# Kernel tuning notes

Hardware: AMD Instinct MI355X
Metric: run time of the kernel (lower is better)

Reference implementation:

```python
import jax, jax.numpy as jnp
import numpy as np

N = 200_000      # nodes
E = 6_400_000    # edges (avg degree 32)
ATT = 16         # scorer hidden dim
MAXD = 512       # mixer max_depth
C = 1.0          # curvature
EPS = 1e-15


def _mobius_add(a, b, c):
    # Mobius addition on the Poincare ball: a (+)_c b
    ab = jnp.sum(a * b, axis=-1, keepdims=True)
    aa = jnp.sum(a * a, axis=-1, keepdims=True)
    bb = jnp.sum(b * b, axis=-1, keepdims=True)
    num = (1.0 + 2.0 * c * ab + c * bb) * a + (1.0 - c * aa) * b
    den = 1.0 + 2.0 * c * ab + (c * c) * aa * bb
    return num / jnp.maximum(den, EPS)


def setup_inputs() -> dict:
    key = jax.random.key(0)
    ks = jax.random.split(key, 8)
    x = jax.random.normal(ks[0], (N, 2), dtype=jnp.float32)
    # keep nodes strictly inside the unit Poincare disk (|x| < 0.5)
    x = 0.5 * x / (1.0 + jnp.linalg.norm(x, axis=-1, keepdims=True))
    edge_index = jax.random.randint(ks[1], (2, E), 0, N, dtype=jnp.int32)
    depth = jax.random.randint(ks[2], (N,), 0, MAXD, dtype=jnp.int32)
    W1 = jax.random.normal(ks[3], (2, ATT), dtype=jnp.float32) * (1.0 / np.sqrt(2.0))
    b1 = jnp.zeros((ATT,), dtype=jnp.float32)
    W2 = jax.random.normal(ks[4], (ATT, 1), dtype=jnp.float32) * (1.0 / np.sqrt(ATT))
    eta = jnp.array(1.0, dtype=jnp.float32)
    depth_scale = 1.0 + 0.1 * jax.random.normal(ks[5], (MAXD, 1), dtype=jnp.float32)
    depth_theta = 0.1 * jax.random.normal(ks[6], (MAXD, 1), dtype=jnp.float32)
    return dict(x=x, edge_index=edge_index, depth=depth, W1=W1, b1=b1, W2=W2,
                eta=eta, depth_scale=depth_scale, depth_theta=depth_theta)


def reference(x, edge_index, depth, W1, b1, W2, eta, depth_scale, depth_theta):
    c = C
    sc = jnp.sqrt(jnp.asarray(c, dtype=x.dtype))
    row, col = edge_index[0], edge_index[1]
    xi = x[row]   # [E,2] target node of each edge
    xj = x[col]   # [E,2] source node of each edge

    # log_{xi}(xj): tangent vector at xi
    u = _mobius_add(-xi, xj, c)                                        # [E,2]
    un = jnp.maximum(jnp.linalg.norm(u, axis=-1, keepdims=True), EPS)  # [E,1]
    lam_i = 2.0 / jnp.maximum(1.0 - c * jnp.sum(xi * xi, axis=-1, keepdims=True), EPS)
    v = (2.0 / (sc * lam_i)) * jnp.arctanh(jnp.minimum(sc * un, 1.0 - 1e-5)) * (u / un)

    # tiny MLP attention score per edge
    h = jax.nn.gelu(v @ W1 + b1, approximate=False)   # [E,ATT]
    scores = (h @ W2)[:, 0]                           # [E]

    # segment softmax over edges grouped by target node `row`
    smax = jax.ops.segment_max(scores, row, num_segments=N)
    ex = jnp.exp(scores - smax[row])
    denom = jax.ops.segment_sum(ex, row, num_segments=N)
    alpha = ex / jnp.maximum(denom[row], 1e-15)       # [E]

    # weighted scatter-add of tangent vectors
    m = jax.ops.segment_sum(alpha[:, None] * v, row, num_segments=N)   # [N,2]

    # depth-gated rotation/scale in the tangent space (mixer)
    d = jnp.clip(depth, 0, MAXD - 1)
    k = depth_scale[d]            # [N,1]
    ang = depth_theta[d][:, 0]    # [N]
    ca, sa = jnp.cos(ang), jnp.sin(ang)
    m = k * jnp.stack([ca * m[:, 0] - sa * m[:, 1],
                       sa * m[:, 0] + ca * m[:, 1]], axis=-1)

    # exp_{x}(eta * m)
    w = eta * m
    wn = jnp.maximum(jnp.linalg.norm(w, axis=-1, keepdims=True), EPS)
    lam_x = 2.0 / jnp.maximum(1.0 - c * jnp.sum(x * x, axis=-1, keepdims=True), EPS)
    second = jnp.tanh(sc * lam_x * wn / 2.0) * (w / (sc * wn))
    return _mobius_add(x, second, c)
```

## Files before the change

kernel.cpp:

```cpp
#include <hip/hip_runtime.h>
#include <hip/hip_fp16.h>
#include <math.h>

#define EPSF 1e-15f
#define BSH  8
#define BSZ  (1 << BSH)
#define BMSK (BSZ - 1)
#define CAPB 9216
#define MAXNB 1024
#define AGG_T 1024
#define KSL   9
#define BIN_T 1024
#define LCH   6400

#define TBL   128
#define TW    129
#define VMIN  (-1.2f)
#define VH    (2.4f / 128.0f)
#define INVH  (128.0f / 2.4f)

__device__ __forceinline__ float fast_rcp(float x)  { return __builtin_amdgcn_rcpf(x); }
__device__ __forceinline__ float fast_rsq(float x)  { return __builtin_amdgcn_rsqf(x); }
__device__ __forceinline__ float fast_exp(float x)  { return __builtin_amdgcn_exp2f(x * 1.4426950408889634f); }

__device__ __forceinline__ unsigned int float_to_ordered(float f) {
    unsigned int u = __float_as_uint(f);
    return (u & 0x80000000u) ? ~u : (u | 0x80000000u);
}
__device__ __forceinline__ float ordered_to_float(unsigned int u) {
    u = (u & 0x80000000u) ? (u & 0x7FFFFFFFu) : ~u;
    return __uint_as_float(u);
}

__device__ __forceinline__ void edge_v_fast(float2 xi, float2 xj, float& vx, float& vy) {
    float ab = -(xi.x * xj.x + xi.y * xj.y);
    float aa = xi.x * xi.x + xi.y * xi.y;
    float bb = xj.x * xj.x + xj.y * xj.y;
    float f1 = 1.0f + 2.0f * ab + bb;
    float f2 = 1.0f - aa;
    float ux = f1 * (-xi.x) + f2 * xj.x;
    float uy = f1 * (-xi.y) + f2 * xj.y;
    float den = 1.0f + 2.0f * ab + aa * bb;
    float inv_den = fast_rcp(fmaxf(den, EPSF));
    ux *= inv_den; uy *= inv_den;
    float un2 = fmaxf(ux * ux + uy * uy, 1e-24f);
    float inv_un = fast_rsq(un2);
    float un = fminf(un2 * inv_un, 1.0f - 1e-5f);
    float t = 0.34657359027997264f * __builtin_amdgcn_logf((1.0f + un) * fast_rcp(1.0f - un));
    float s = fmaxf(f2, EPSF) * t * inv_un;
    vx = s * ux; vy = s * uy;
}

__device__ __forceinline__ void edge_v(float2 xi, float2 xj, float& vx, float& vy) {
    float ab = -(xi.x * xj.x + xi.y * xj.y);
    float aa = xi.x * xi.x + xi.y * xi.y;
    float bb = xj.x * xj.x + xj.y * xj.y;
    float f1 = 1.0f + 2.0f * ab + bb;
    float f2 = 1.0f - aa;
    float ux = f1 * (-xi.x) + f2 * xj.x;
    float uy = f1 * (-xi.y) + f2 * xj.y;
    float den = 1.0f + 2.0f * ab + aa * bb;
    float inv_den = 1.0f / fmaxf(den, EPSF);
    ux *= inv_den; uy *= inv_den;
    float un = fmaxf(sqrtf(ux * ux + uy * uy), EPSF);
    float t  = atanhf(fminf(un, 1.0f - 1e-5f));
    float s = fmaxf(f2, EPSF) * t / un;
    vx = s * ux; vy = s * uy;
}

__device__ __forceinline__ float edge_score(float vx, float vy,
                                            const float* __restrict__ W1,
                                            const float* __restrict__ b1,
                                            const float* __restrict__ W2) {
    float score = 0.0f;
#pragma unroll
    for (int k = 0; k < 16; ++k) {
        float z = fmaf(vx, W1[k], fmaf(vy, W1[16 + k], b1[k]));
        float g = 0.5f * z * (1.0f + erff(z * 0.70710678118654752f));
        score = fmaf(g, W2[k], score);
    }
    return score;
}

__device__ __forceinline__ float2 finalize_node(float2 xv, float mx, float my,
                                                int d, float eta,
                                                const float* __restrict__ dscale,
                                                const float* __restrict__ dtheta) {
    d = d < 0 ? 0 : (d > 511 ? 511 : d);
    float k   = dscale[d];
    float ang = dtheta[d];
    float ca = cosf(ang), sa = sinf(ang);
    float m0 = k * (ca * mx - sa * my);
    float m1 = k * (sa * mx + ca * my);

    float wx = eta * m0, wy = eta * m1;
    float wn = fmaxf(sqrtf(wx * wx + wy * wy), 1e-15f);

    float aa = xv.x * xv.x + xv.y * xv.y;
    float lam = 2.0f / fmaxf(1.0f - aa, 1e-15f);
    float fac = tanhf(lam * wn * 0.5f) / wn;
    float sx = fac * wx, sy = fac * wy;

    float ab = xv.x * sx + xv.y * sy;
    float bb = sx * sx + sy * sy;
    float n1 = 1.0f + 2.0f * ab + bb;
    float n2 = 1.0f - aa;
    float ox = n1 * xv.x + n2 * sx;
    float oy = n1 * xv.y + n2 * sy;
    float dd = 1.0f + 2.0f * ab + aa * bb;
    float inv = 1.0f / fmaxf(dd, 1e-15f);
    return make_float2(ox * inv, oy * inv);
}


__global__ void init_cursor(unsigned* __restrict__ cursor, int NB) {
    int b = blockIdx.x * blockDim.x + threadIdx.x;
    if (b < NB) cursor[b] = (unsigned)b * CAPB;
}

__global__ void build_score_table(const float* __restrict__ W1,
                                  const float* __restrict__ b1,
                                  const float* __restrict__ W2,
                                  float* __restrict__ tbl) {
    int i = blockIdx.x * blockDim.x + threadIdx.x;
    if (i >= TW * TW) return;
    int iy = i / TW, ix = i - iy * TW;
    float vx = VMIN + VH * (float)ix;
    float vy = VMIN + VH * (float)iy;
    tbl[i] = edge_score(vx, vy, W1, b1, W2);
}

__global__ __launch_bounds__(BIN_T)
void bin_edges(const int* __restrict__ ei,
               unsigned* __restrict__ cursor,
               unsigned* __restrict__ sorted,
               int E, int NB) {
    __shared__ unsigned bkrank[LCH];
    __shared__ unsigned payload[LCH];
    __shared__ unsigned sortedLoc[LCH];
    __shared__ unsigned gdst[LCH];
    __shared__ unsigned hist[MAXNB];
    __shared__ unsigned scanA[MAXNB];
    __shared__ unsigned loc[MAXNB];
    __shared__ unsigned gbase[MAXNB];

    int tid = threadIdx.x;
    int e0 = blockIdx.x * LCH;
    int cnt = min(E - e0, LCH);
    if (cnt <= 0) return;

    if (tid < MAXNB) hist[tid] = 0;
    __syncthreads();

    for (int idx = tid; idx < cnt; idx += BIN_T) {
        int r = ei[e0 + idx];
        int c = ei[E + e0 + idx];
        unsigned bk = (unsigned)r >> BSH;
        unsigned rank = atomicAdd(&hist[bk], 1u);
        bkrank[idx] = (bk << 14) | rank;
        payload[idx] = ((unsigned)(r & BMSK) << 24) | (unsigned)c;
    }
    __syncthreads();

    unsigned h = (tid < MAXNB) ? hist[tid] : 0u;
    if (tid < MAXNB) scanA[tid] = h;
    __syncthreads();
#pragma unroll
    for (int step = 1; step < MAXNB; step <<= 1) {
        unsigned v = 0u;
        if (tid < MAXNB) {
            v = scanA[tid];
            if (tid >= step) v += scanA[tid - step];
        }
        __syncthreads();
        if (tid < MAXNB) scanA[tid] = v;
        __syncthreads();
    }
    if (tid < MAXNB) {
        loc[tid] = scanA[tid] - h;
        gbase[tid] = h ? atomicAdd(&cursor[tid], h) : 0u;
    }
    __syncthreads();

    for (int idx = tid; idx < cnt; idx += BIN_T) {
        unsigned v = bkrank[idx];
        unsigned bk = v >> 14;
        unsigned rank = v & 0x3FFFu;
        unsigned pos = loc[bk] + rank;
        sortedLoc[pos] = payload[idx];
        unsigned g = gbase[bk] + rank;
        gdst[pos] = (g < (bk + 1u) * CAPB) ? g : 0xFFFFFFFFu;
    }
    __syncthreads();

    for (int idx = tid; idx < cnt; idx += BIN_T) {
        unsigned g = gdst[idx];
        if (g != 0xFFFFFFFFu) sorted[g] = sortedLoc[idx];
    }
}

__global__ __launch_bounds__(AGG_T, 8)
void aggregate(const float2* __restrict__ x,
               const unsigned* __restrict__ cursor,
               const unsigned* __restrict__ sorted,
               const int* __restrict__ depth,
               const float* __restrict__ tbl,
               const float* __restrict__ etaPtr,
               const float* __restrict__ dscale,
               const float* __restrict__ dtheta,
               float2* __restrict__ out, int N) {
    __shared__ float2 xr[BSZ];
    __shared__ unsigned nmax[BSZ];
    __shared__ unsigned long long accP[BSZ];

    int b = blockIdx.x;
    int tid = threadIdx.x;
    int nb0 = b << BSH;
    int nodeCnt = min(BSZ, N - nb0);
    if (tid < BSZ) {
        nmax[tid] = 0u;
        accP[tid] = 0ull;
        if (tid < nodeCnt) xr[tid] = x[nb0 + tid];
    }
    __syncthreads();

    unsigned basep = (unsigned)b * CAPB;
    unsigned cnt = cursor[b] - basep;
    cnt = cnt > (unsigned)CAPB ? (unsigned)CAPB : cnt;
    const unsigned* __restrict__ sb = sorted + basep;

    unsigned u[KSL];
#pragma unroll
    for (int k = 0; k < KSL; ++k) {
        u[k] = sb[(unsigned)tid + (unsigned)(k * AGG_T)];
    }

    int rl[KSL];
    float2 xj[KSL];
#pragma unroll
    for (int k = 0; k < KSL; ++k) {
        unsigned i = (unsigned)tid + (unsigned)(k * AGG_T);
        bool act = i < cnt;
        rl[k] = (int)(u[k] >> 24);
        int c = act ? (int)(u[k] & 0xFFFFFFu) : 0;
        xj[k] = x[c];
    }

    unsigned pkA[KSL];
    unsigned pkV[KSL];
#pragma unroll
    for (int k = 0; k < KSL; ++k) {
        unsigned i = (unsigned)tid + (unsigned)(k * AGG_T);
        bool act = i < cnt;
        float2 xi = xr[rl[k]];
        float vx, vy;
        edge_v_fast(xi, xj[k], vx, vy);

        float tx = fminf(fmaxf((vx - VMIN) * INVH, 0.0f), 127.999f);
        float ty = fminf(fmaxf((vy - VMIN) * INVH, 0.0f), 127.999f);
        int ix = (int)tx, iy = (int)ty;
        float fx = tx - (float)ix, fy = ty - (float)iy;
        const float* row = tbl + iy * TW + ix;
        float s00 = row[0], s01 = row[1];
        float s10 = row[TW], s11 = row[TW + 1];
        float sA = fmaf(fx, s01 - s00, s00);
        float sB = fmaf(fx, s11 - s10, s10);
        float score = fmaf(fy, sB - sA, sA);

        __half hs = __float2half_rn(score);
        float sq = __half2float(hs);
        unsigned short s16 = *(unsigned short*)&hs;
        __half2 h2 = __floats2half2_rn(vx, vy);
        pkA[k] = ((unsigned)rl[k] << 16) | (unsigned)s16;
        pkV[k] = *(unsigned*)&h2;
        if (act) atomicMax(&nmax[rl[k]], float_to_ordered(sq));
    }
    __syncthreads();

#pragma unroll
    for (int k = 0; k < KSL; ++k) {
        unsigned i = (unsigned)tid + (unsigned)(k * AGG_T);
        if (i >= cnt) continue;
        int rlk = (int)(pkA[k] >> 16);
        unsigned short s16 = (unsigned short)(pkA[k] & 0xFFFFu);
        __half hs = *(__half*)&s16;
        float s = __half2float(hs);
        float mxs = ordered_to_float(nmax[rlk]);
        float ex = fast_exp(s - mxs);
        __half2 h2 = *(__half2*)&pkV[k];
        float2 v2 = __half22float2(h2);
        unsigned e0 = __float2uint_rn(ex * 16384.0f);
        unsigned e1 = __float2uint_rn(ex * (v2.x + 2.0f) * 0.25f * 16384.0f);
        unsigned e2 = __float2uint_rn(ex * (v2.y + 2.0f) * 0.25f * 16384.0f);
        unsigned long long pk = (unsigned long long)e0
                              | ((unsigned long long)e1 << 21)
                              | ((unsigned long long)e2 << 42);
        atomicAdd(&accP[rlk], pk);
    }
    __syncthreads();

    if (tid >= nodeCnt) return;
    unsigned long long w = accP[tid];
    float F0 = (float)(unsigned int)(w & 0x1FFFFFull);
    float F1 = (float)(unsigned int)((w >> 21) & 0x1FFFFFull);
    float F2 = (float)(unsigned int)(w >> 42);
    float mx = 0.0f, my = 0.0f;
    if (F0 > 0.0f) {
        float inv = 1.0f / F0;
        mx = 4.0f * F1 * inv - 2.0f;
        my = 4.0f * F2 * inv - 2.0f;
    }
    int i = nb0 + tid;
    out[i] = finalize_node(xr[tid], mx, my, depth[i], etaPtr[0], dscale, dtheta);
}


__global__ void init_kernel(unsigned int* __restrict__ smax,
                            unsigned long long* __restrict__ maccP, int N) {
    int i = blockIdx.x * blockDim.x + threadIdx.x;
    if (i < N) {
        smax[i] = float_to_ordered(-INFINITY);
        maccP[i] = 0ull;
    }
}

__global__ void pass1_score_max(const float2* __restrict__ x,
                                const int* __restrict__ ei,
                                const float* __restrict__ W1,
                                const float* __restrict__ b1,
                                const float* __restrict__ W2,
                                unsigned int* __restrict__ smax, int E) {
    int e = blockIdx.x * blockDim.x + threadIdx.x;
    if (e >= E) return;
    int r = ei[e];
    int c = ei[E + e];
    float vx, vy;
    edge_v(x[r], x[c], vx, vy);
    float score = edge_score(vx, vy, W1, b1, W2);
    atomicMax(&smax[r], float_to_ordered(score));
}

#define PK_SCALE 16384.0f

__global__ void pass2_accum(const float2* __restrict__ x,
                            const int* __restrict__ ei,
                            const float* __restrict__ W1,
                            const float* __restrict__ b1,
                            const float* __restrict__ W2,
                            const unsigned int* __restrict__ smax,
                            unsigned long long* __restrict__ maccP, int E) {
    int e = blockIdx.x * blockDim.x + threadIdx.x;
    if (e >= E) return;
    int r = ei[e];
    int c = ei[E + e];
    float vx, vy;
    edge_v(x[r], x[c], vx, vy);
    float score = edge_score(vx, vy, W1, b1, W2);
    float mx = ordered_to_float(smax[r]);
    float ex = expf(score - mx);
    unsigned e0 = __float2uint_rn(ex * PK_SCALE);
    unsigned e1 = __float2uint_rn(ex * (vx + 2.0f) * 0.25f * PK_SCALE);
    unsigned e2 = __float2uint_rn(ex * (vy + 2.0f) * 0.25f * PK_SCALE);
    unsigned long long pk = (unsigned long long)e0
                          | ((unsigned long long)e1 << 21)
                          | ((unsigned long long)e2 << 42);
    atomicAdd(&maccP[r], pk);
}

__global__ void pass3_finalize(const float2* __restrict__ x,
                               const int* __restrict__ depth,
                               const unsigned long long* __restrict__ maccP,
                               const float* __restrict__ etaPtr,
                               const float* __restrict__ dscale,
                               const float* __restrict__ dtheta,
                               float2* __restrict__ out, int N) {
    int i = blockIdx.x * blockDim.x + threadIdx.x;
    if (i >= N) return;
    unsigned long long w = maccP[i];
    float F0 = (float)(unsigned int)(w & 0x1FFFFFull);
    float F1 = (float)(unsigned int)((w >> 21) & 0x1FFFFFull);
    float F2 = (float)(unsigned int)(w >> 42);
    float mx = 0.0f, my = 0.0f;
    if (F0 > 0.0f) {
        float inv = 1.0f / F0;
        mx = 4.0f * F1 * inv - 2.0f;
        my = 4.0f * F2 * inv - 2.0f;
    }
    out[i] = finalize_node(x[i], mx, my, depth[i], etaPtr[0], dscale, dtheta);
}


extern "C" void kernel_launch(void* const* d_in, const int* in_sizes, int n_in,
                              void* d_out, int out_size, void* d_ws, size_t ws_size,
                              hipStream_t stream) {
    const float2* x   = (const float2*)d_in[0];
    const int* ei     = (const int*)d_in[1];
    const int* depth  = (const int*)d_in[2];
    const float* W1   = (const float*)d_in[3];
    const float* b1   = (const float*)d_in[4];
    const float* W2   = (const float*)d_in[5];
    const float* eta  = (const float*)d_in[6];
    const float* dsc  = (const float*)d_in[7];
    const float* dth  = (const float*)d_in[8];
    float2* out = (float2*)d_out;

    int N = in_sizes[0] / 2;
    int E = in_sizes[1] / 2;
    int NB = (N + BSZ - 1) >> BSH;

    const int B = 256;
    size_t sortedBytes = (size_t)NB * CAPB * 4;
    size_t need = 4096 + sortedBytes + (size_t)TW * TW * 4;
    if (NB <= MAXNB && ws_size >= need) {
        unsigned* cursor = (unsigned*)d_ws;
        unsigned* sorted = (unsigned*)((char*)d_ws + 4096);
        float* tbl = (float*)((char*)d_ws + 4096 + sortedBytes);
        int binG = (E + LCH - 1) / LCH;
        init_cursor<<<(NB + B - 1) / B, B, 0, stream>>>(cursor, NB);
        build_score_table<<<(TW * TW + B - 1) / B, B, 0, stream>>>(W1, b1, W2, tbl);
        bin_edges<<<binG, BIN_T, 0, stream>>>(ei, cursor, sorted, E, NB);
        aggregate<<<NB, AGG_T, 0, stream>>>(x, cursor, sorted, depth, tbl,
                                            eta, dsc, dth, out, N);
    } else {
        unsigned long long* maccP = (unsigned long long*)d_ws;
        unsigned int* smax = (unsigned int*)(maccP + N);
        init_kernel<<<(N + B - 1) / B, B, 0, stream>>>(smax, maccP, N);
        pass1_score_max<<<(E + B - 1) / B, B, 0, stream>>>(x, ei, W1, b1, W2, smax, E);
        pass2_accum<<<(E + B - 1) / B, B, 0, stream>>>(x, ei, W1, b1, W2, smax, maccP, E);
        pass3_finalize<<<(N + B - 1) / B, B, 0, stream>>>(x, depth, maccP, eta, dsc, dth, out, N);
    }
}
```

Measured before the change: 193.0 us.

## Stage score table in LDS, wave-shuffle bucket scan, smaller binning chunks

The aggregate kernel now copies the 129x129 score table into shared memory per block and issues the sorted-edge loads before the table copy and first barrier. This moves the bilinear lookups from global memory to LDS and overlaps load latency with setup. The binning kernel replaces its 10-step shared-memory Hillis-Steele scan, which needed a barrier per step, with a wave-level shuffle scan plus a 16-entry cross-wave scan. Its chunk size drops to 4096 edges with a launch-bounds occupancy hint, giving more blocks and less LDS per block. In exchange, aggregate uses about 66KB more LDS per block, which may lower occupancy, and the per-block table copy adds global traffic.

```diff
diff --git a/kernel.cpp b/kernel.cpp
--- a/kernel.cpp
+++ b/kernel.cpp
@@ -11,10 +11,11 @@
 #define AGG_T 1024
 #define KSL   9
 #define BIN_T 1024
-#define LCH   6400
+#define LCH   4096
 
 #define TBL   128
 #define TW    129
+#define TWSZ  (TW * TW)
 #define VMIN  (-1.2f)
 #define VH    (2.4f / 128.0f)
 #define INVH  (128.0f / 2.4f)
@@ -123,14 +124,14 @@
                                   const float* __restrict__ W2,
                                   float* __restrict__ tbl) {
     int i = blockIdx.x * blockDim.x + threadIdx.x;
-    if (i >= TW * TW) return;
+    if (i >= TWSZ) return;
     int iy = i / TW, ix = i - iy * TW;
     float vx = VMIN + VH * (float)ix;
     float vy = VMIN + VH * (float)iy;
     tbl[i] = edge_score(vx, vy, W1, b1, W2);
 }
 
-__global__ __launch_bounds__(BIN_T)
+__global__ __launch_bounds__(BIN_T, 8)
 void bin_edges(const int* __restrict__ ei,
                unsigned* __restrict__ cursor,
                unsigned* __restrict__ sorted,
@@ -140,16 +141,16 @@
     __shared__ unsigned sortedLoc[LCH];
     __shared__ unsigned gdst[LCH];
     __shared__ unsigned hist[MAXNB];
-    __shared__ unsigned scanA[MAXNB];
     __shared__ unsigned loc[MAXNB];
     __shared__ unsigned gbase[MAXNB];
+    __shared__ unsigned waveSum[16];
 
     int tid = threadIdx.x;
     int e0 = blockIdx.x * LCH;
     int cnt = min(E - e0, LCH);
     if (cnt <= 0) return;
 
-    if (tid < MAXNB) hist[tid] = 0;
+    hist[tid] = 0;
     __syncthreads();
 
     for (int idx = tid; idx < cnt; idx += BIN_T) {
@@ -162,30 +163,36 @@
     }
     __syncthreads();
 
-    unsigned h = (tid < MAXNB) ? hist[tid] : 0u;
-    if (tid < MAXNB) scanA[tid] = h;
-    __syncthreads();
-#pragma unroll
-    for (int step = 1; step < MAXNB; step <<= 1) {
-        unsigned v = 0u;
-        if (tid < MAXNB) {
-            v = scanA[tid];
-            if (tid >= step) v += scanA[tid - step];
+    unsigned h = hist[tid];
+    unsigned v = h;
+    int lane = tid & 63;
+    int wv = tid >> 6;
+#pragma unroll
+    for (int s = 1; s < 64; s <<= 1) {
+        unsigned t = __shfl_up(v, s, 64);
+        if (lane >= s) v += t;
+    }
+    if (lane == 63) waveSum[wv] = v;
+    __syncthreads();
+    if (wv == 0) {
+        unsigned w2 = (lane < 16) ? waveSum[lane] : 0u;
+#pragma unroll
+        for (int s = 1; s < 16; s <<= 1) {
+            unsigned t = __shfl_up(w2, s, 64);
+            if (lane >= s) w2 += t;
         }
-        __syncthreads();
-        if (tid < MAXNB) scanA[tid] = v;
-        __syncthreads();
-    }
-    if (tid < MAXNB) {
-        loc[tid] = scanA[tid] - h;
-        gbase[tid] = h ? atomicAdd(&cursor[tid], h) : 0u;
-    }
+        if (lane < 16) waveSum[lane] = w2;
+    }
+    __syncthreads();
+    unsigned base = wv ? waveSum[wv - 1] : 0u;
+    loc[tid] = base + v - h;
+    gbase[tid] = h ? atomicAdd(&cursor[tid], h) : 0u;
     __syncthreads();
 
     for (int idx = tid; idx < cnt; idx += BIN_T) {
-        unsigned v = bkrank[idx];
-        unsigned bk = v >> 14;
-        unsigned rank = v & 0x3FFFu;
+        unsigned w = bkrank[idx];
+        unsigned bk = w >> 14;
+        unsigned rank = w & 0x3FFFu;
         unsigned pos = loc[bk] + rank;
         sortedLoc[pos] = payload[idx];
         unsigned g = gbase[bk] + rank;
@@ -209,6 +216,7 @@
                const float* __restrict__ dscale,
                const float* __restrict__ dtheta,
                float2* __restrict__ out, int N) {
+    __shared__ float tl[TWSZ];
     __shared__ float2 xr[BSZ];
     __shared__ unsigned nmax[BSZ];
     __shared__ unsigned long long accP[BSZ];
@@ -217,42 +225,45 @@
     int tid = threadIdx.x;
     int nb0 = b << BSH;
     int nodeCnt = min(BSZ, N - nb0);
+
+    unsigned basep = (unsigned)b * CAPB;
+    const unsigned* __restrict__ sb = sorted + basep;
+
+    unsigned u[KSL];
+#pragma unroll
+    for (int k = 0; k < KSL; ++k) {
+        u[k] = sb[(unsigned)tid + (unsigned)(k * AGG_T)];
+    }
+    __builtin_amdgcn_sched_barrier(0);
+
+    for (int i = tid; i < TWSZ; i += AGG_T) tl[i] = tbl[i];
     if (tid < BSZ) {
         nmax[tid] = 0u;
         accP[tid] = 0ull;
         if (tid < nodeCnt) xr[tid] = x[nb0 + tid];
     }
-    __syncthreads();
-
-    unsigned basep = (unsigned)b * CAPB;
+
     unsigned cnt = cursor[b] - basep;
     cnt = cnt > (unsigned)CAPB ? (unsigned)CAPB : cnt;
-    const unsigned* __restrict__ sb = sorted + basep;
-
-    unsigned u[KSL];
+
+    float2 xj[KSL];
 #pragma unroll
     for (int k = 0; k < KSL; ++k) {
-        u[k] = sb[(unsigned)tid + (unsigned)(k * AGG_T)];
-    }
-
-    int rl[KSL];
-    float2 xj[KSL];
+        unsigned i = (unsigned)tid + (unsigned)(k * AGG_T);
+        int c = (i < cnt) ? (int)(u[k] & 0xFFFFFFu) : 0;
+        xj[k] = x[c];
+    }
+    __builtin_amdgcn_sched_barrier(0);
+    __syncthreads();
+
+    unsigned pkA[KSL];
+    unsigned pkV[KSL];
 #pragma unroll
     for (int k = 0; k < KSL; ++k) {
         unsigned i = (unsigned)tid + (unsigned)(k * AGG_T);
         bool act = i < cnt;
-        rl[k] = (int)(u[k] >> 24);
-        int c = act ? (int)(u[k] & 0xFFFFFFu) : 0;
-        xj[k] = x[c];
-    }
-
-    unsigned pkA[KSL];
-    unsigned pkV[KSL];
-#pragma unroll
-    for (int k = 0; k < KSL; ++k) {
-        unsigned i = (unsigned)tid + (unsigned)(k * AGG_T);
-        bool act = i < cnt;
-        float2 xi = xr[rl[k]];
+        int rl = (int)(u[k] >> 24);
+        float2 xi = xr[rl];
         float vx, vy;
         edge_v_fast(xi, xj[k], vx, vy);
 
@@ -260,7 +271,7 @@
         float ty = fminf(fmaxf((vy - VMIN) * INVH, 0.0f), 127.999f);
         int ix = (int)tx, iy = (int)ty;
         float fx = tx - (float)ix, fy = ty - (float)iy;
-        const float* row = tbl + iy * TW + ix;
+        const float* row = tl + iy * TW + ix;
         float s00 = row[0], s01 = row[1];
         float s10 = row[TW], s11 = row[TW + 1];
         float sA = fmaf(fx, s01 - s00, s00);
@@ -271,9 +282,9 @@
         float sq = __half2float(hs);
         unsigned short s16 = *(unsigned short*)&hs;
         __half2 h2 = __floats2half2_rn(vx, vy);
-        pkA[k] = ((unsigned)rl[k] << 16) | (unsigned)s16;
+        pkA[k] = ((unsigned)rl << 16) | (unsigned)s16;
         pkV[k] = *(unsigned*)&h2;
-        if (act) atomicMax(&nmax[rl[k]], float_to_ordered(sq));
+        if (act) atomicMax(&nmax[rl], float_to_ordered(sq));
     }
     __syncthreads();
 
@@ -410,14 +421,14 @@
 
     const int B = 256;
     size_t sortedBytes = (size_t)NB * CAPB * 4;
-    size_t need = 4096 + sortedBytes + (size_t)TW * TW * 4;
+    size_t need = 4096 + sortedBytes + (size_t)TWSZ * 4;
     if (NB <= MAXNB && ws_size >= need) {
         unsigned* cursor = (unsigned*)d_ws;
         unsigned* sorted = (unsigned*)((char*)d_ws + 4096);
         float* tbl = (float*)((char*)d_ws + 4096 + sortedBytes);
         int binG = (E + LCH - 1) / LCH;
         init_cursor<<<(NB + B - 1) / B, B, 0, stream>>>(cursor, NB);
-        build_score_table<<<(TW * TW + B - 1) / B, B, 0, stream>>>(W1, b1, W2, tbl);
+        build_score_table<<<(TWSZ + B - 1) / B, B, 0, stream>>>(W1, b1, W2, tbl);
         bin_edges<<<binG, BIN_T, 0, stream>>>(ei, cursor, sorted, E, NB);
         aggregate<<<NB, AGG_T, 0, stream>>>(x, cursor, sorted, depth, tbl,
                                             eta, dsc, dth, out, N);
```

Result: faster. 186.6 us (-3.3%).
